# Kernel tuning notes

Hardware: AMD Instinct MI355X
Metric: run time of the kernel (lower is better)

Reference implementation:

```python
import jax, jax.numpy as jnp
import numpy as np

EMBED_DIM = 512
N_HEAD = 8
Q_DIM = 64
V_DIM = 64
WINDOW_SIZE = 3


def setup_inputs() -> dict:
    key = jax.random.key(0)
    ks = jax.random.split(key, 9)
    B, N = 2, 2048
    x = jax.random.normal(ks[0], (B, N, EMBED_DIM), dtype=jnp.float32)
    s = 0.02
    # torch nn.Linear weights are [out_features, in_features]; y = x @ W.T + b
    Wq = jax.random.normal(ks[1], (N_HEAD * Q_DIM, EMBED_DIM), dtype=jnp.float32) * s
    bq = jax.random.normal(ks[2], (N_HEAD * Q_DIM,), dtype=jnp.float32) * s
    Wk = jax.random.normal(ks[3], (N_HEAD * Q_DIM, EMBED_DIM), dtype=jnp.float32) * s
    bk = jax.random.normal(ks[4], (N_HEAD * Q_DIM,), dtype=jnp.float32) * s
    Wv = jax.random.normal(ks[5], (N_HEAD * V_DIM, EMBED_DIM), dtype=jnp.float32) * s
    bv = jax.random.normal(ks[6], (N_HEAD * V_DIM,), dtype=jnp.float32) * s
    Wo = jax.random.normal(ks[7], (EMBED_DIM, N_HEAD * V_DIM), dtype=jnp.float32) * s
    bo = jax.random.normal(ks[8], (EMBED_DIM,), dtype=jnp.float32) * s
    return {"x": x, "Wq": Wq, "bq": bq, "Wk": Wk, "bk": bk,
            "Wv": Wv, "bv": bv, "Wo": Wo, "bo": bo}


def _diag_indices(n_seq, di):
    # rows i and cols j = i + di of the di-th diagonal
    if di >= 0:
        ii = np.arange(0, n_seq - di)
    else:
        ii = np.arange(-di, n_seq)
    return ii, ii + di


def reference(x, Wq, bq, Wk, bk, Wv, bv, Wo, bo):
    B, N, E = x.shape
    H, Dq, Dv = N_HEAD, Q_DIM, V_DIM
    Q = (x @ Wq.T + bq).reshape(B, N, H, Dq).transpose(0, 2, 1, 3)  # [B,H,N,Dq]
    K = (x @ Wk.T + bk).reshape(B, N, H, Dq).transpose(0, 2, 1, 3)
    V = (x @ Wv.T + bv).reshape(B, N, H, Dv).transpose(0, 2, 1, 3)  # [B,H,N,Dv]
    half = WINDOW_SIZE // 2
    # Faithful to source: scores scattered into COLUMN index i (the loop
    # counter), not the key position; all other columns remain 0 and still
    # participate in the full softmax over n_seq.
    columns = jnp.zeros((B, H, N, N), dtype=x.dtype)
    for i, di in enumerate(range(-half, half + 1)):
        ii, jj = _diag_indices(N, di)
        c = jnp.einsum('bhid,bhid->bhi', Q[:, :, ii, :], K[:, :, jj, :])
        columns = columns.at[:, :, ii, i].set(c)
    attn = jax.nn.softmax(columns, axis=-1)          # [B,H,N,N]
    out = attn @ V                                    # [B,H,N,Dv]
    out = out.transpose(0, 2, 1, 3).reshape(B, N, H * Dv)
    return out @ Wo.T + bo
```

## Files before the change

kernel.cpp:

```cpp
#include <hip/hip_runtime.h>
#include <hip/hip_bf16.h>

#define EMBED 512
#define NH 8
#define DH 64
#define NSEQ 2048
#define BATCH 2
#define NROWS (BATCH * NSEQ)
#define QKV_STRIDE 1536

typedef unsigned short u16;
typedef __bf16 bf16x8 __attribute__((ext_vector_type(8)));
typedef float f32x4 __attribute__((ext_vector_type(4)));

__device__ __forceinline__ u16 f2bf(float f) {
    unsigned u = __float_as_uint(f);
    unsigned r = (u + 0x7FFFu + ((u >> 16) & 1u)) >> 16;
    return (u16)r;
}

#define XELEMS   (NROWS * EMBED)
#define WCATELEMS (1536 * EMBED)
#define WOELEMS  (EMBED * EMBED)

__global__ __launch_bounds__(256) void prep_kernel(
    const float* __restrict__ x,
    const float* __restrict__ Wq, const float* __restrict__ Wk,
    const float* __restrict__ Wv, const float* __restrict__ Wo,
    u16* __restrict__ xb, u16* __restrict__ Wcat, u16* __restrict__ Wob)
{
    const long long e0 = (long long)(blockIdx.x * 256 + threadIdx.x) * 8;
    const float* src;
    u16* dst;
    if (e0 < XELEMS) {
        src = x + e0; dst = xb + e0;
    } else if (e0 < XELEMS + WCATELEMS) {
        const long long j = e0 - XELEMS;
        const int row = (int)(j >> 9);
        const int col = (int)(j & 511);
        const int sel = row >> 9;
        const int r   = row & 511;
        const float* W = (sel == 0) ? Wq : (sel == 1) ? Wk : Wv;
        src = W + (size_t)r * EMBED + col; dst = Wcat + j;
    } else {
        const long long j = e0 - XELEMS - WCATELEMS;
        src = Wo + j; dst = Wob + j;
    }
    float4 a = *(const float4*)(src);
    float4 b = *(const float4*)(src + 4);
    union { u16 u[8]; uint4 v; } p;
    p.u[0] = f2bf(a.x); p.u[1] = f2bf(a.y); p.u[2] = f2bf(a.z); p.u[3] = f2bf(a.w);
    p.u[4] = f2bf(b.x); p.u[5] = f2bf(b.y); p.u[6] = f2bf(b.z); p.u[7] = f2bf(b.w);
    *(uint4*)(dst) = p.v;
}

__device__ __forceinline__ void gemm_tile_128(
    const u16* __restrict__ A, const u16* __restrict__ W,
    const float* __restrict__ bias,
    float* __restrict__ C, int ldc, int m0, int n0w, int n0c)
{
    __shared__ u16 As[128 * 32];
    __shared__ u16 Bs[128 * 32];

    const int t    = threadIdx.x;
    const int wave = t >> 6, lane = t & 63;
    const int wm   = wave >> 1, wn = wave & 1;
    const int qd   = lane >> 4, lr = lane & 15;

    f32x4 acc[4][4] = {};

    const u16* Ag = A + (size_t)m0 * EMBED;
    const u16* Wg = W + (size_t)n0w * EMBED;
    const int srow = t >> 2;
    const int sk   = (t & 3) * 8;

    u16* AsW0 = As + (size_t)(wave * 64) * 8;
    u16* AsW1 = As + (size_t)(256 + wave * 64) * 8;
    u16* BsW0 = Bs + (size_t)(wave * 64) * 8;
    u16* BsW1 = Bs + (size_t)(256 + wave * 64) * 8;

    for (int kc = 0; kc < EMBED; kc += 32) {
        __builtin_amdgcn_global_load_lds(
            (const __attribute__((address_space(1))) void*)(Ag + (size_t)srow * EMBED + kc + sk),
            (__attribute__((address_space(3))) void*)AsW0, 16, 0, 0);
        __builtin_amdgcn_global_load_lds(
            (const __attribute__((address_space(1))) void*)(Ag + (size_t)(srow + 64) * EMBED + kc + sk),
            (__attribute__((address_space(3))) void*)AsW1, 16, 0, 0);
        __builtin_amdgcn_global_load_lds(
            (const __attribute__((address_space(1))) void*)(Wg + (size_t)srow * EMBED + kc + sk),
            (__attribute__((address_space(3))) void*)BsW0, 16, 0, 0);
        __builtin_amdgcn_global_load_lds(
            (const __attribute__((address_space(1))) void*)(Wg + (size_t)(srow + 64) * EMBED + kc + sk),
            (__attribute__((address_space(3))) void*)BsW1, 16, 0, 0);
        __syncthreads();

        bf16x8 af[4], bfr[4];
#pragma unroll
        for (int i = 0; i < 4; ++i) {
            af[i]  = *(const bf16x8*)&As[(wm * 64 + i * 16 + lr) * 32 + qd * 8];
            bfr[i] = *(const bf16x8*)&Bs[(wn * 64 + i * 16 + lr) * 32 + qd * 8];
        }
#pragma unroll
        for (int mi = 0; mi < 4; ++mi)
#pragma unroll
            for (int ni = 0; ni < 4; ++ni)
                acc[mi][ni] = __builtin_amdgcn_mfma_f32_16x16x32_bf16(
                    af[mi], bfr[ni], acc[mi][ni], 0, 0, 0);
        __syncthreads();
    }

#pragma unroll
    for (int ni = 0; ni < 4; ++ni) {
        const int cl = wn * 64 + ni * 16 + lr;
        const float bv = bias[cl];
        const int col = n0c + cl;
#pragma unroll
        for (int mi = 0; mi < 4; ++mi) {
#pragma unroll
            for (int e = 0; e < 4; ++e) {
                const int row = m0 + wm * 64 + mi * 16 + qd * 4 + e;
                C[(size_t)row * ldc + col] = acc[mi][ni][e] + bv;
            }
        }
    }
}

__global__ __launch_bounds__(256) void gemm_qkv_mfma(
    const u16* __restrict__ xb, const u16* __restrict__ Wcat,
    const float* __restrict__ bq, const float* __restrict__ bk,
    const float* __restrict__ bv, float* __restrict__ QKV)
{
    const int m0 = blockIdx.x * 128;
    const int n0 = blockIdx.y * 128;
    const int sel = n0 >> 9;
    const float* bias = ((sel == 0) ? bq : (sel == 1) ? bk : bv) + (n0 & 511);
    gemm_tile_128(xb, Wcat, bias, QKV, QKV_STRIDE, m0, n0, n0);
}

__global__ __launch_bounds__(256) void gemm_out_mfma(
    const u16* __restrict__ AOb, const u16* __restrict__ Wob,
    const float* __restrict__ bo, float* __restrict__ C)
{
    const int m0 = blockIdx.x * 128;
    const int n0 = blockIdx.y * 128;
    gemm_tile_128(AOb, Wob, bo + n0, C, EMBED, m0, n0, n0);
}

__global__ __launch_bounds__(256) void vsum_part(
    const float* __restrict__ QKV, float* __restrict__ vpart)
{
    const int bh = blockIdx.x;
    const int b = bh >> 3, h = bh & 7;
    const int wave = threadIdx.x >> 6, lane = threadIdx.x & 63;
    const float* Vb = QKV + (size_t)(b * NSEQ) * QKV_STRIDE + 1024 + h * DH + lane;
    const int j0 = blockIdx.y * 256 + wave * 64;
    float s = 0.f;
#pragma unroll 8
    for (int j = j0; j < j0 + 64; ++j) s += Vb[(size_t)j * QKV_STRIDE];
    vpart[(size_t)(bh * 32 + blockIdx.y * 4 + wave) * 64 + lane] = s;
}

__global__ __launch_bounds__(256) void attn_kernel(
    const float* __restrict__ QKV, const float* __restrict__ vpart,
    u16* __restrict__ AOb)
{
    const int bh = blockIdx.x;
    const int b = bh >> 3, h = bh & 7;
    const int wave = threadIdx.x >> 6, lane = threadIdx.x & 63;

    const float* Qb = QKV + (size_t)(b * NSEQ) * QKV_STRIDE + h * DH;
    const float* Kb = Qb + 512;
    const float* Vb = Qb + 1024;

    const float v0 = Vb[(size_t)0 * QKV_STRIDE + lane];
    const float v1 = Vb[(size_t)1 * QKV_STRIDE + lane];
    const float v2 = Vb[(size_t)2 * QKV_STRIDE + lane];
    float vs = 0.f;
#pragma unroll
    for (int c = 0; c < 32; ++c) vs += vpart[(size_t)(bh * 32 + c) * 64 + lane];
    vs -= (v0 + v1 + v2);

    u16* AObh = AOb + (size_t)(b * NSEQ) * EMBED + h * DH;
    const int r0 = blockIdx.y * 16 + wave * 4;

#pragma unroll
    for (int i = 0; i < 4; ++i) {
        const int r = r0 + i;
        const float q  = Qb[(size_t)r * QKV_STRIDE + lane];
        const float km = Kb[(size_t)r * QKV_STRIDE + lane];
        const float kp = (r > 0)        ? Kb[(size_t)(r - 1) * QKV_STRIDE + lane] : 0.f;
        const float kn = (r < NSEQ - 1) ? Kb[(size_t)(r + 1) * QKV_STRIDE + lane] : 0.f;
        float s0 = q * kp, s1 = q * km, s2 = q * kn;
#pragma unroll
        for (int off = 32; off > 0; off >>= 1) {
            s0 += __shfl_xor(s0, off);
            s1 += __shfl_xor(s1, off);
            s2 += __shfl_xor(s2, off);
        }
        const float m  = fmaxf(fmaxf(s0, s1), fmaxf(s2, 0.f));
        const float e0 = __expf(s0 - m);
        const float e1 = __expf(s1 - m);
        const float e2 = __expf(s2 - m);
        const float eb = __expf(-m);
        const float rd = 1.f / (e0 + e1 + e2 + (float)(NSEQ - 3) * eb);
        const float o  = (e0 * v0 + e1 * v1 + e2 * v2 + eb * vs) * rd;
        AObh[(size_t)r * EMBED + lane] = f2bf(o);
    }
}

extern "C" void kernel_launch(void* const* d_in, const int* in_sizes, int n_in,
                              void* d_out, int out_size, void* d_ws, size_t ws_size,
                              hipStream_t stream)
{
    const float* x  = (const float*)d_in[0];
    const float* Wq = (const float*)d_in[1];
    const float* bq = (const float*)d_in[2];
    const float* Wk = (const float*)d_in[3];
    const float* bk = (const float*)d_in[4];
    const float* Wv = (const float*)d_in[5];
    const float* bv = (const float*)d_in[6];
    const float* Wo = (const float*)d_in[7];
    const float* bo = (const float*)d_in[8];
    float* out = (float*)d_out;

    float* QKV  = (float*)d_ws;
    u16*   xb   = (u16*)(QKV + (size_t)NROWS * QKV_STRIDE);
    u16*   AOb  = xb;
    u16*   Wcat = xb + XELEMS;
    u16*   Wob  = Wcat + WCATELEMS;
    float* vpart = (float*)(Wob + WOELEMS);

    const int prep_blocks = (XELEMS + WCATELEMS + WOELEMS) / 8 / 256;
    prep_kernel<<<prep_blocks, 256, 0, stream>>>(x, Wq, Wk, Wv, Wo, xb, Wcat, Wob);
    gemm_qkv_mfma<<<dim3(32, 12), 256, 0, stream>>>(xb, Wcat, bq, bk, bv, QKV);
    vsum_part<<<dim3(16, 8), 256, 0, stream>>>(QKV, vpart);
    attn_kernel<<<dim3(16, 128), 256, 0, stream>>>(QKV, vpart, AOb);
    gemm_out_mfma<<<dim3(32, 4), 256, 0, stream>>>(AOb, Wob, bo, out);
}
```

Before: 123.9 us.

## Fuse V column sums into QKV GEMM epilogue and halve output GEMM tile width

Drops the separate vsum_part kernel. The QKV GEMM blocks that produce V columns now reduce their accumulators per column into a partial-sum buffer, and the attention kernel adds the bias term N*bv back in. This saves a launch and a full re-read of V from global memory, at the cost of an extra shared-memory reduction and sync in the GEMM epilogue. Separately, the output GEMM uses 128x64 tiles, doubling its grid from 128 to 256 blocks to fill more CUs.

```diff
diff --git a/kernel.cpp b/kernel.cpp
--- a/kernel.cpp
+++ b/kernel.cpp
@@ -57,10 +57,12 @@
 __device__ __forceinline__ void gemm_tile_128(
     const u16* __restrict__ A, const u16* __restrict__ W,
     const float* __restrict__ bias,
-    float* __restrict__ C, int ldc, int m0, int n0w, int n0c)
+    float* __restrict__ C, int ldc, int m0, int n0w, int n0c,
+    float* __restrict__ vpartial, int mblock)
 {
     __shared__ u16 As[128 * 32];
     __shared__ u16 Bs[128 * 32];
+    __shared__ float csum[2][128];
 
     const int t    = threadIdx.x;
     const int wave = t >> 6, lane = t & 63;
@@ -123,50 +125,115 @@
             }
         }
     }
+
+    if (vpartial) {
+#pragma unroll
+        for (int ni = 0; ni < 4; ++ni) {
+            float s = 0.f;
+#pragma unroll
+            for (int mi = 0; mi < 4; ++mi)
+#pragma unroll
+                for (int e = 0; e < 4; ++e) s += acc[mi][ni][e];
+            s += __shfl_xor(s, 16);
+            s += __shfl_xor(s, 32);
+            if (qd == 0) csum[wm][wn * 64 + ni * 16 + lr] = s;
+        }
+        __syncthreads();
+        if (t < 128)
+            vpartial[(size_t)t * 32 + mblock] = csum[0][t] + csum[1][t];
+    }
 }
 
 __global__ __launch_bounds__(256) void gemm_qkv_mfma(
     const u16* __restrict__ xb, const u16* __restrict__ Wcat,
     const float* __restrict__ bq, const float* __restrict__ bk,
-    const float* __restrict__ bv, float* __restrict__ QKV)
+    const float* __restrict__ bv, float* __restrict__ QKV,
+    float* __restrict__ vpart2)
 {
     const int m0 = blockIdx.x * 128;
     const int n0 = blockIdx.y * 128;
     const int sel = n0 >> 9;
     const float* bias = ((sel == 0) ? bq : (sel == 1) ? bk : bv) + (n0 & 511);
-    gemm_tile_128(xb, Wcat, bias, QKV, QKV_STRIDE, m0, n0, n0);
+    float* vp = (sel == 2) ? (vpart2 + (size_t)(n0 - 1024) * 32) : nullptr;
+    gemm_tile_128(xb, Wcat, bias, QKV, QKV_STRIDE, m0, n0, n0, vp, blockIdx.x);
 }
 
 __global__ __launch_bounds__(256) void gemm_out_mfma(
-    const u16* __restrict__ AOb, const u16* __restrict__ Wob,
+    const u16* __restrict__ A, const u16* __restrict__ W,
     const float* __restrict__ bo, float* __restrict__ C)
 {
+    __shared__ u16 As[128 * 32];
+    __shared__ u16 Bs[64 * 32];
+
     const int m0 = blockIdx.x * 128;
-    const int n0 = blockIdx.y * 128;
-    gemm_tile_128(AOb, Wob, bo + n0, C, EMBED, m0, n0, n0);
-}
-
-__global__ __launch_bounds__(256) void vsum_part(
-    const float* __restrict__ QKV, float* __restrict__ vpart)
+    const int n0 = blockIdx.y * 64;
+
+    const int t    = threadIdx.x;
+    const int wave = t >> 6, lane = t & 63;
+    const int wm   = wave >> 1, wn = wave & 1;
+    const int qd   = lane >> 4, lr = lane & 15;
+
+    f32x4 acc[4][2] = {};
+
+    const u16* Ag = A + (size_t)m0 * EMBED;
+    const u16* Wg = W + (size_t)n0 * EMBED;
+    const int srow = t >> 2;
+    const int sk   = (t & 3) * 8;
+
+    u16* AsW0 = As + (size_t)(wave * 64) * 8;
+    u16* AsW1 = As + (size_t)(256 + wave * 64) * 8;
+    u16* BsW0 = Bs + (size_t)(wave * 64) * 8;
+
+    for (int kc = 0; kc < EMBED; kc += 32) {
+        __builtin_amdgcn_global_load_lds(
+            (const __attribute__((address_space(1))) void*)(Ag + (size_t)srow * EMBED + kc + sk),
+            (__attribute__((address_space(3))) void*)AsW0, 16, 0, 0);
+        __builtin_amdgcn_global_load_lds(
+            (const __attribute__((address_space(1))) void*)(Ag + (size_t)(srow + 64) * EMBED + kc + sk),
+            (__attribute__((address_space(3))) void*)AsW1, 16, 0, 0);
+        __builtin_amdgcn_global_load_lds(
+            (const __attribute__((address_space(1))) void*)(Wg + (size_t)srow * EMBED + kc + sk),
+            (__attribute__((address_space(3))) void*)BsW0, 16, 0, 0);
+        __syncthreads();
+
+        bf16x8 af[4], bfr[2];
+#pragma unroll
+        for (int i = 0; i < 4; ++i)
+            af[i]  = *(const bf16x8*)&As[(wm * 64 + i * 16 + lr) * 32 + qd * 8];
+#pragma unroll
+        for (int i = 0; i < 2; ++i)
+            bfr[i] = *(const bf16x8*)&Bs[(wn * 32 + i * 16 + lr) * 32 + qd * 8];
+#pragma unroll
+        for (int mi = 0; mi < 4; ++mi)
+#pragma unroll
+            for (int ni = 0; ni < 2; ++ni)
+                acc[mi][ni] = __builtin_amdgcn_mfma_f32_16x16x32_bf16(
+                    af[mi], bfr[ni], acc[mi][ni], 0, 0, 0);
+        __syncthreads();
+    }
+
+#pragma unroll
+    for (int ni = 0; ni < 2; ++ni) {
+        const int cl = wn * 32 + ni * 16 + lr;
+        const float bv = bo[n0 + cl];
+#pragma unroll
+        for (int mi = 0; mi < 4; ++mi) {
+#pragma unroll
+            for (int e = 0; e < 4; ++e) {
+                const int row = m0 + wm * 64 + mi * 16 + qd * 4 + e;
+                C[(size_t)row * EMBED + n0 + cl] = acc[mi][ni][e] + bv;
+            }
+        }
+    }
+}
+
+__global__ __launch_bounds__(256) void attn_kernel(
+    const float* __restrict__ QKV, const float* __restrict__ vpart2,
+    const float* __restrict__ bvv, u16* __restrict__ AOb)
 {
     const int bh = blockIdx.x;
     const int b = bh >> 3, h = bh & 7;
     const int wave = threadIdx.x >> 6, lane = threadIdx.x & 63;
-    const float* Vb = QKV + (size_t)(b * NSEQ) * QKV_STRIDE + 1024 + h * DH + lane;
-    const int j0 = blockIdx.y * 256 + wave * 64;
-    float s = 0.f;
-#pragma unroll 8
-    for (int j = j0; j < j0 + 64; ++j) s += Vb[(size_t)j * QKV_STRIDE];
-    vpart[(size_t)(bh * 32 + blockIdx.y * 4 + wave) * 64 + lane] = s;
-}
-
-__global__ __launch_bounds__(256) void attn_kernel(
-    const float* __restrict__ QKV, const float* __restrict__ vpart,
-    u16* __restrict__ AOb)
-{
-    const int bh = blockIdx.x;
-    const int b = bh >> 3, h = bh & 7;
-    const int wave = threadIdx.x >> 6, lane = threadIdx.x & 63;
 
     const float* Qb = QKV + (size_t)(b * NSEQ) * QKV_STRIDE + h * DH;
     const float* Kb = Qb + 512;
@@ -175,9 +242,13 @@
     const float v0 = Vb[(size_t)0 * QKV_STRIDE + lane];
     const float v1 = Vb[(size_t)1 * QKV_STRIDE + lane];
     const float v2 = Vb[(size_t)2 * QKV_STRIDE + lane];
+
+    const int c = h * DH + lane;
     float vs = 0.f;
 #pragma unroll
-    for (int c = 0; c < 32; ++c) vs += vpart[(size_t)(bh * 32 + c) * 64 + lane];
+    for (int mb = 0; mb < 16; ++mb)
+        vs += vpart2[(size_t)c * 32 + b * 16 + mb];
+    vs += (float)NSEQ * bvv[c];
     vs -= (v0 + v1 + v2);
 
     u16* AObh = AOb + (size_t)(b * NSEQ) * EMBED + h * DH;
@@ -228,12 +299,11 @@
     u16*   AOb  = xb;
     u16*   Wcat = xb + XELEMS;
     u16*   Wob  = Wcat + WCATELEMS;
-    float* vpart = (float*)(Wob + WOELEMS);
+    float* vpart2 = (float*)(Wob + WOELEMS);
 
     const int prep_blocks = (XELEMS + WCATELEMS + WOELEMS) / 8 / 256;
     prep_kernel<<<prep_blocks, 256, 0, stream>>>(x, Wq, Wk, Wv, Wo, xb, Wcat, Wob);
-    gemm_qkv_mfma<<<dim3(32, 12), 256, 0, stream>>>(xb, Wcat, bq, bk, bv, QKV);
-    vsum_part<<<dim3(16, 8), 256, 0, stream>>>(QKV, vpart);
-    attn_kernel<<<dim3(16, 128), 256, 0, stream>>>(QKV, vpart, AOb);
-    gemm_out_mfma<<<dim3(32, 4), 256, 0, stream>>>(AOb, Wob, bo, out);
-}
+    gemm_qkv_mfma<<<dim3(32, 12), 256, 0, stream>>>(xb, Wcat, bq, bk, bv, QKV, vpart2);
+    attn_kernel<<<dim3(16, 128), 256, 0, stream>>>(QKV, vpart2, bv, AOb);
+    gemm_out_mfma<<<dim3(32, 8), 256, 0, stream>>>(AOb, Wob, bo, out);
+}
```

Result: faster. 114.0 us (-8.0%).

## Fuse QKV GEMM, attention and output GEMM into one persistent kernel with grid barriers

Applied to the files above, without the earlier changes.

Merges the QKV projection, V column-sum, attention and output projection into a single 768-block kernel separated by software grid barriers. The barrier counters are reset in the prep kernel. GEMM tiles shrink to 128x64 so there are enough blocks to fill the grid. The V column sums are now taken from the GEMM accumulators in the epilogue, with bias added analytically, which removes the separate vsum pass. This saves kernel launch gaps and the re-read of V, but relies on all 768 blocks being co-resident and adds spin-wait barrier cost.

```diff
diff --git a/kernel.cpp b/kernel.cpp
--- a/kernel.cpp
+++ b/kernel.cpp
@@ -2,12 +2,10 @@
 #include <hip/hip_bf16.h>
 
 #define EMBED 512
-#define NH 8
-#define DH 64
 #define NSEQ 2048
-#define BATCH 2
-#define NROWS (BATCH * NSEQ)
+#define NROWS 4096
 #define QKV_STRIDE 1536
+#define NBLK 768
 
 typedef unsigned short u16;
 typedef __bf16 bf16x8 __attribute__((ext_vector_type(8)));
@@ -19,16 +17,19 @@
     return (u16)r;
 }
 
-#define XELEMS   (NROWS * EMBED)
+#define XELEMS    (NROWS * EMBED)
 #define WCATELEMS (1536 * EMBED)
-#define WOELEMS  (EMBED * EMBED)
+#define WOELEMS   (EMBED * EMBED)
 
 __global__ __launch_bounds__(256) void prep_kernel(
     const float* __restrict__ x,
     const float* __restrict__ Wq, const float* __restrict__ Wk,
     const float* __restrict__ Wv, const float* __restrict__ Wo,
-    u16* __restrict__ xb, u16* __restrict__ Wcat, u16* __restrict__ Wob)
-{
+    u16* __restrict__ xb, u16* __restrict__ Wcat, u16* __restrict__ Wob,
+    unsigned* __restrict__ bar)
+{
+    if (blockIdx.x == 0 && threadIdx.x < 2) bar[threadIdx.x] = 0;
+
     const long long e0 = (long long)(blockIdx.x * 256 + threadIdx.x) * 8;
     const float* src;
     u16* dst;
@@ -54,30 +55,41 @@
     *(uint4*)(dst) = p.v;
 }
 
-__device__ __forceinline__ void gemm_tile_128(
+__device__ __forceinline__ void grid_barrier(unsigned* ctr)
+{
+    __syncthreads();
+    if (threadIdx.x == 0) {
+        __threadfence();
+        __hip_atomic_fetch_add(ctr, 1u, __ATOMIC_RELEASE, __HIP_MEMORY_SCOPE_AGENT);
+        while (__hip_atomic_load(ctr, __ATOMIC_ACQUIRE, __HIP_MEMORY_SCOPE_AGENT) < NBLK)
+            __builtin_amdgcn_s_sleep(8);
+    }
+    __syncthreads();
+    __threadfence();
+}
+
+__device__ __forceinline__ void gemm_tile_128x64(
+    u16* __restrict__ As, u16* __restrict__ Bs, float (*csum)[64],
     const u16* __restrict__ A, const u16* __restrict__ W,
     const float* __restrict__ bias,
-    float* __restrict__ C, int ldc, int m0, int n0w, int n0c)
-{
-    __shared__ u16 As[128 * 32];
-    __shared__ u16 Bs[128 * 32];
-
+    float* __restrict__ C, int ldc, int m0, int n0,
+    float* __restrict__ vpartial, int mblock)
+{
     const int t    = threadIdx.x;
     const int wave = t >> 6, lane = t & 63;
     const int wm   = wave >> 1, wn = wave & 1;
     const int qd   = lane >> 4, lr = lane & 15;
-
-    f32x4 acc[4][4] = {};
-
-    const u16* Ag = A + (size_t)m0 * EMBED;
-    const u16* Wg = W + (size_t)n0w * EMBED;
     const int srow = t >> 2;
     const int sk   = (t & 3) * 8;
+
+    f32x4 acc[4][2] = {};
+
+    const u16* Ag = A + (size_t)m0 * EMBED;
+    const u16* Wg = W + (size_t)n0 * EMBED;
 
     u16* AsW0 = As + (size_t)(wave * 64) * 8;
     u16* AsW1 = As + (size_t)(256 + wave * 64) * 8;
     u16* BsW0 = Bs + (size_t)(wave * 64) * 8;
-    u16* BsW1 = Bs + (size_t)(256 + wave * 64) * 8;
 
     for (int kc = 0; kc < EMBED; kc += 32) {
         __builtin_amdgcn_global_load_lds(
@@ -89,122 +101,138 @@
         __builtin_amdgcn_global_load_lds(
             (const __attribute__((address_space(1))) void*)(Wg + (size_t)srow * EMBED + kc + sk),
             (__attribute__((address_space(3))) void*)BsW0, 16, 0, 0);
-        __builtin_amdgcn_global_load_lds(
-            (const __attribute__((address_space(1))) void*)(Wg + (size_t)(srow + 64) * EMBED + kc + sk),
-            (__attribute__((address_space(3))) void*)BsW1, 16, 0, 0);
-        __syncthreads();
-
-        bf16x8 af[4], bfr[4];
-#pragma unroll
-        for (int i = 0; i < 4; ++i) {
+        __syncthreads();
+
+        bf16x8 af[4], bfr[2];
+#pragma unroll
+        for (int i = 0; i < 4; ++i)
             af[i]  = *(const bf16x8*)&As[(wm * 64 + i * 16 + lr) * 32 + qd * 8];
-            bfr[i] = *(const bf16x8*)&Bs[(wn * 64 + i * 16 + lr) * 32 + qd * 8];
-        }
+#pragma unroll
+        for (int i = 0; i < 2; ++i)
+            bfr[i] = *(const bf16x8*)&Bs[(wn * 32 + i * 16 + lr) * 32 + qd * 8];
 #pragma unroll
         for (int mi = 0; mi < 4; ++mi)
 #pragma unroll
-            for (int ni = 0; ni < 4; ++ni)
+            for (int ni = 0; ni < 2; ++ni)
                 acc[mi][ni] = __builtin_amdgcn_mfma_f32_16x16x32_bf16(
                     af[mi], bfr[ni], acc[mi][ni], 0, 0, 0);
         __syncthreads();
     }
 
 #pragma unroll
-    for (int ni = 0; ni < 4; ++ni) {
-        const int cl = wn * 64 + ni * 16 + lr;
-        const float bv = bias[cl];
-        const int col = n0c + cl;
+    for (int ni = 0; ni < 2; ++ni) {
+        const int cl = wn * 32 + ni * 16 + lr;
+        const float bb = bias[cl];
 #pragma unroll
         for (int mi = 0; mi < 4; ++mi) {
 #pragma unroll
             for (int e = 0; e < 4; ++e) {
                 const int row = m0 + wm * 64 + mi * 16 + qd * 4 + e;
-                C[(size_t)row * ldc + col] = acc[mi][ni][e] + bv;
+                C[(size_t)row * ldc + n0 + cl] = acc[mi][ni][e] + bb;
             }
         }
     }
-}
-
-__global__ __launch_bounds__(256) void gemm_qkv_mfma(
+
+    if (vpartial) {
+#pragma unroll
+        for (int ni = 0; ni < 2; ++ni) {
+            float s = 0.f;
+#pragma unroll
+            for (int mi = 0; mi < 4; ++mi)
+#pragma unroll
+                for (int e = 0; e < 4; ++e) s += acc[mi][ni][e];
+            s += __shfl_xor(s, 16);
+            s += __shfl_xor(s, 32);
+            if (qd == 0) csum[wm][wn * 32 + ni * 16 + lr] = s;
+        }
+        __syncthreads();
+        if (t < 64)
+            vpartial[(size_t)t * 32 + mblock] = csum[0][t] + csum[1][t];
+        __syncthreads();
+    }
+}
+
+__global__ __launch_bounds__(256, 3) void mega_kernel(
     const u16* __restrict__ xb, const u16* __restrict__ Wcat,
+    const u16* __restrict__ Wob,
     const float* __restrict__ bq, const float* __restrict__ bk,
-    const float* __restrict__ bv, float* __restrict__ QKV)
-{
-    const int m0 = blockIdx.x * 128;
-    const int n0 = blockIdx.y * 128;
-    const int sel = n0 >> 9;
-    const float* bias = ((sel == 0) ? bq : (sel == 1) ? bk : bv) + (n0 & 511);
-    gemm_tile_128(xb, Wcat, bias, QKV, QKV_STRIDE, m0, n0, n0);
-}
-
-__global__ __launch_bounds__(256) void gemm_out_mfma(
-    const u16* __restrict__ AOb, const u16* __restrict__ Wob,
-    const float* __restrict__ bo, float* __restrict__ C)
-{
-    const int m0 = blockIdx.x * 128;
-    const int n0 = blockIdx.y * 128;
-    gemm_tile_128(AOb, Wob, bo + n0, C, EMBED, m0, n0, n0);
-}
-
-__global__ __launch_bounds__(256) void vsum_part(
-    const float* __restrict__ QKV, float* __restrict__ vpart)
-{
-    const int bh = blockIdx.x;
-    const int b = bh >> 3, h = bh & 7;
-    const int wave = threadIdx.x >> 6, lane = threadIdx.x & 63;
-    const float* Vb = QKV + (size_t)(b * NSEQ) * QKV_STRIDE + 1024 + h * DH + lane;
-    const int j0 = blockIdx.y * 256 + wave * 64;
-    float s = 0.f;
-#pragma unroll 8
-    for (int j = j0; j < j0 + 64; ++j) s += Vb[(size_t)j * QKV_STRIDE];
-    vpart[(size_t)(bh * 32 + blockIdx.y * 4 + wave) * 64 + lane] = s;
-}
-
-__global__ __launch_bounds__(256) void attn_kernel(
-    const float* __restrict__ QKV, const float* __restrict__ vpart,
-    u16* __restrict__ AOb)
-{
-    const int bh = blockIdx.x;
-    const int b = bh >> 3, h = bh & 7;
-    const int wave = threadIdx.x >> 6, lane = threadIdx.x & 63;
-
-    const float* Qb = QKV + (size_t)(b * NSEQ) * QKV_STRIDE + h * DH;
-    const float* Kb = Qb + 512;
-    const float* Vb = Qb + 1024;
-
-    const float v0 = Vb[(size_t)0 * QKV_STRIDE + lane];
-    const float v1 = Vb[(size_t)1 * QKV_STRIDE + lane];
-    const float v2 = Vb[(size_t)2 * QKV_STRIDE + lane];
-    float vs = 0.f;
-#pragma unroll
-    for (int c = 0; c < 32; ++c) vs += vpart[(size_t)(bh * 32 + c) * 64 + lane];
-    vs -= (v0 + v1 + v2);
-
-    u16* AObh = AOb + (size_t)(b * NSEQ) * EMBED + h * DH;
-    const int r0 = blockIdx.y * 16 + wave * 4;
-
-#pragma unroll
-    for (int i = 0; i < 4; ++i) {
-        const int r = r0 + i;
-        const float q  = Qb[(size_t)r * QKV_STRIDE + lane];
-        const float km = Kb[(size_t)r * QKV_STRIDE + lane];
-        const float kp = (r > 0)        ? Kb[(size_t)(r - 1) * QKV_STRIDE + lane] : 0.f;
-        const float kn = (r < NSEQ - 1) ? Kb[(size_t)(r + 1) * QKV_STRIDE + lane] : 0.f;
-        float s0 = q * kp, s1 = q * km, s2 = q * kn;
-#pragma unroll
-        for (int off = 32; off > 0; off >>= 1) {
-            s0 += __shfl_xor(s0, off);
-            s1 += __shfl_xor(s1, off);
-            s2 += __shfl_xor(s2, off);
+    const float* __restrict__ bv, const float* __restrict__ bo,
+    float* __restrict__ QKV, float* __restrict__ vpart2,
+    u16* __restrict__ AOb, float* __restrict__ out,
+    unsigned* __restrict__ bar)
+{
+    __shared__ __align__(16) u16 As[128 * 32];
+    __shared__ __align__(16) u16 Bs[64 * 32];
+    __shared__ float csum[2][64];
+
+    {
+        const int m0 = (blockIdx.x & 31) * 128;
+        const int n0 = (blockIdx.x >> 5) * 64;
+        const int sel = n0 >> 9;
+        const float* bias = ((sel == 0) ? bq : (sel == 1) ? bk : bv) + (n0 & 511);
+        float* vp = (sel == 2) ? (vpart2 + (size_t)(n0 - 1024) * 32) : nullptr;
+        gemm_tile_128x64(As, Bs, csum, xb, Wcat, bias, QKV, QKV_STRIDE,
+                         m0, n0, vp, m0 >> 7);
+    }
+    grid_barrier(bar + 0);
+
+    {
+        const int wave = threadIdx.x >> 6, lane = threadIdx.x & 63;
+        const int gw = blockIdx.x * 4 + wave;
+        for (int task = gw; task < 8192; task += NBLK * 4) {
+            const int bh = task >> 9;
+            const int r0 = (task & 511) * 4;
+            const int b = bh >> 3, h = bh & 7;
+
+            const float* Qb = QKV + (size_t)(b * NSEQ) * QKV_STRIDE + h * 64;
+            const float* Kb = Qb + 512;
+            const float* Vb = Qb + 1024;
+
+            const float v0 = Vb[(size_t)0 * QKV_STRIDE + lane];
+            const float v1 = Vb[(size_t)1 * QKV_STRIDE + lane];
+            const float v2 = Vb[(size_t)2 * QKV_STRIDE + lane];
+
+            const int c = h * 64 + lane;
+            float vs = 0.f;
+#pragma unroll
+            for (int mb = 0; mb < 16; ++mb)
+                vs += vpart2[(size_t)c * 32 + b * 16 + mb];
+            vs += (float)NSEQ * bv[c];
+            vs -= (v0 + v1 + v2);
+
+            u16* AObh = AOb + (size_t)(b * NSEQ) * EMBED + h * 64;
+#pragma unroll
+            for (int i = 0; i < 4; ++i) {
+                const int r = r0 + i;
+                const float q  = Qb[(size_t)r * QKV_STRIDE + lane];
+                const float km = Kb[(size_t)r * QKV_STRIDE + lane];
+                const float kp = (r > 0)        ? Kb[(size_t)(r - 1) * QKV_STRIDE + lane] : 0.f;
+                const float kn = (r < NSEQ - 1) ? Kb[(size_t)(r + 1) * QKV_STRIDE + lane] : 0.f;
+                float s0 = q * kp, s1 = q * km, s2 = q * kn;
+#pragma unroll
+                for (int off = 32; off > 0; off >>= 1) {
+                    s0 += __shfl_xor(s0, off);
+                    s1 += __shfl_xor(s1, off);
+                    s2 += __shfl_xor(s2, off);
+                }
+                const float m  = fmaxf(fmaxf(s0, s1), fmaxf(s2, 0.f));
+                const float e0 = __expf(s0 - m);
+                const float e1 = __expf(s1 - m);
+                const float e2 = __expf(s2 - m);
+                const float eb = __expf(-m);
+                const float rd = 1.f / (e0 + e1 + e2 + (float)(NSEQ - 3) * eb);
+                const float o  = (e0 * v0 + e1 * v1 + e2 * v2 + eb * vs) * rd;
+                AObh[(size_t)r * EMBED + lane] = f2bf(o);
+            }
         }
-        const float m  = fmaxf(fmaxf(s0, s1), fmaxf(s2, 0.f));
-        const float e0 = __expf(s0 - m);
-        const float e1 = __expf(s1 - m);
-        const float e2 = __expf(s2 - m);
-        const float eb = __expf(-m);
-        const float rd = 1.f / (e0 + e1 + e2 + (float)(NSEQ - 3) * eb);
-        const float o  = (e0 * v0 + e1 * v1 + e2 * v2 + eb * vs) * rd;
-        AObh[(size_t)r * EMBED + lane] = f2bf(o);
+    }
+    grid_barrier(bar + 1);
+
+    if (blockIdx.x < 256) {
+        const int m0 = (blockIdx.x >> 3) * 128;
+        const int n0 = (blockIdx.x & 7) * 64;
+        gemm_tile_128x64(As, Bs, csum, AOb, Wob, bo + n0, out, EMBED,
+                         m0, n0, nullptr, 0);
     }
 }
 
@@ -223,17 +251,16 @@
     const float* bo = (const float*)d_in[8];
     float* out = (float*)d_out;
 
-    float* QKV  = (float*)d_ws;
-    u16*   xb   = (u16*)(QKV + (size_t)NROWS * QKV_STRIDE);
-    u16*   AOb  = xb;
-    u16*   Wcat = xb + XELEMS;
-    u16*   Wob  = Wcat + WCATELEMS;
-    float* vpart = (float*)(Wob + WOELEMS);
+    float*   QKV    = (float*)d_ws;
+    u16*     xb     = (u16*)(QKV + (size_t)NROWS * QKV_STRIDE);
+    u16*     AOb    = xb;
+    u16*     Wcat   = xb + XELEMS;
+    u16*     Wob    = Wcat + WCATELEMS;
+    float*   vpart2 = (float*)(Wob + WOELEMS);
+    unsigned* bar   = (unsigned*)(vpart2 + 512 * 32);
 
     const int prep_blocks = (XELEMS + WCATELEMS + WOELEMS) / 8 / 256;
-    prep_kernel<<<prep_blocks, 256, 0, stream>>>(x, Wq, Wk, Wv, Wo, xb, Wcat, Wob);
-    gemm_qkv_mfma<<<dim3(32, 12), 256, 0, stream>>>(xb, Wcat, bq, bk, bv, QKV);
-    vsum_part<<<dim3(16, 8), 256, 0, stream>>>(QKV, vpart);
-    attn_kernel<<<dim3(16, 128), 256, 0, stream>>>(QKV, vpart, AOb);
-    gemm_out_mfma<<<dim3(32, 4), 256, 0, stream>>>(AOb, Wob, bo, out);
-}
+    prep_kernel<<<prep_blocks, 256, 0, stream>>>(x, Wq, Wk, Wv, Wo, xb, Wcat, Wob, bar);
+    mega_kernel<<<NBLK, 256, 0, stream>>>(xb, Wcat, Wob, bq, bk, bv, bo,
+                                          QKV, vpart2, AOb, out, bar);
+}
```

Measured after the change: 393.9 us. +217.8%, slower.
